# Optimization experiments

Hardware: AMD Instinct MI355X
Metric: run time of the kernel (lower is better)

## Reference

```python
import jax, jax.numpy as jnp
import numpy as np

DIM_IN, DIM_K, DIM_V = 1024, 1024, 1024

def setup_inputs() -> dict:
    key = jax.random.key(0)
    k1, k2, k3, k4 = jax.random.split(key, 4)
    x = jax.random.normal(k1, (4, 2048, DIM_IN), dtype=jnp.float32)
    # Linear(dim_in, dim_k, bias=False): store as [in, out] for x @ W
    Wq = jax.random.normal(k2, (DIM_IN, DIM_K), dtype=jnp.float32) * (1.0 / np.sqrt(DIM_IN))
    Wk = jax.random.normal(k3, (DIM_IN, DIM_K), dtype=jnp.float32) * (1.0 / np.sqrt(DIM_IN))
    Wv = jax.random.normal(k4, (DIM_IN, DIM_V), dtype=jnp.float32) * (1.0 / np.sqrt(DIM_IN))
    return {"x": x, "Wq": Wq, "Wk": Wk, "Wv": Wv, "causal_mask": 1}

def reference(x, Wq, Wk, Wv, causal_mask):
    # x: [b, n, dim_in]
    b, n, _ = x.shape
    q = jnp.einsum('bnd,dk->bnk', x, Wq)
    k = jnp.einsum('bnd,dk->bnk', x, Wk)
    v = jnp.einsum('bnd,dv->bnv', x, Wv)
    scale = 1.0 / np.sqrt(Wq.shape[1])
    dist = jnp.einsum('bik,bjk->bij', q, k) * scale  # [b, n, n]
    if causal_mask:
        mask = jnp.tril(jnp.ones((n, n), dtype=bool))
        dist = jnp.where(mask, dist, -jnp.inf)
    attn = jax.nn.softmax(dist, axis=-1)
    return jnp.einsum('bij,bjv->biv', attn, v)  # [b, n, dim_v]
```

## Files before the change

### kernel.cpp

```cpp
#include <hip/hip_runtime.h>
#include <hip/hip_bf16.h>
#include <stdint.h>

#define BM 128
#define BN 128
#define BK 64

typedef __attribute__((ext_vector_type(8))) short bf16x8;
typedef __attribute__((ext_vector_type(4))) float floatx4;


__device__ __forceinline__ unsigned short f2bf(float f) {
    unsigned int x;
    __builtin_memcpy(&x, &f, 4);
    unsigned int r = (x + 0x7fffu + ((x >> 16) & 1u)) >> 16;
    return (unsigned short)r;
}

__device__ __forceinline__ float bf2f_hi(unsigned int u_hi_masked) {
    float f;
    __builtin_memcpy(&f, &u_hi_masked, 4);
    return f;
}

__device__ __forceinline__ void async_copy16(const void* g, void* l) {
    __builtin_amdgcn_global_load_lds(
        (const __attribute__((address_space(1))) void*)(uintptr_t)g,
        (__attribute__((address_space(3))) void*)(uint32_t)(uintptr_t)l,
        16, 0, 0);
}


__global__ __launch_bounds__(256) void prep(const float* __restrict__ x,
                                            const float* __restrict__ Wq,
                                            const float* __restrict__ Wk,
                                            const float* __restrict__ Wv,
                                            unsigned short* __restrict__ xb,
                                            unsigned short* __restrict__ wT) {
    __shared__ float tile[32][33];
    int bid = blockIdx.x;
    int tid = threadIdx.x;
    if (bid < 8192) {
        int i = bid * 256 + tid;
        float4 v = ((const float4*)x)[i];
        ushort4 o;
        o.x = f2bf(v.x);
        o.y = f2bf(v.y);
        o.z = f2bf(v.z);
        o.w = f2bf(v.w);
        ((ushort4*)xb)[i] = o;
    } else {
        int w = bid - 8192;
        int z = w >> 10;
        int r = w & 1023;
        int bx = (r & 31) * 32;
        int by = (r >> 5) * 32;
        const float* W = z == 0 ? Wq : (z == 1 ? Wk : Wv);
        int tx = tid & 31, ty = tid >> 5;
        for (int rr = 0; rr < 32; rr += 8)
            tile[ty + rr][tx] = W[(size_t)(by + ty + rr) * 1024 + bx + tx];
        __syncthreads();
        unsigned short* o = wT + (size_t)z * 1024 * 1024;
        for (int rr = 0; rr < 32; rr += 8)
            o[(size_t)(bx + ty + rr) * 1024 + by + tx] = f2bf(tile[tx][ty + rr]);
    }
}


#define SEG_STRIDE 544
#define BUF_SH (16 * SEG_STRIDE)


__device__ __forceinline__ void gemm_core(const unsigned short* __restrict__ A,
                                          int lda,
                                          const unsigned short* __restrict__ B,
                                          int ldb, void* __restrict__ C,
                                          int ldc, bool out_bf16, int kend,
                                          float scale, int m0, int n0) {
    __shared__ __align__(16) unsigned short As[BUF_SH];
    __shared__ __align__(16) unsigned short Bs[BUF_SH];

    int tid = threadIdx.x;
    int lane = tid & 63;
    int wave = tid >> 6;
    int wm = (wave >> 1) * 64;
    int wn = (wave & 1) * 64;
    int fr = lane & 15;
    int kq = lane >> 4;

    floatx4 acc[4][4] = {};

    for (int k0 = 0; k0 < kend; k0 += BK) {
#pragma unroll
        for (int q = 0; q < 4; q++) {
            int s = 4 * q + wave;
            int r = s * 8 + (lane >> 3);
            int ko = (lane & 7) * 8;
            int dst = s * SEG_STRIDE + lane * 8;
            async_copy16(A + (size_t)(m0 + r) * lda + k0 + ko, &As[dst]);
            async_copy16(B + (size_t)(n0 + r) * ldb + k0 + ko, &Bs[dst]);
        }
        __syncthreads();

#pragma unroll
        for (int kh = 0; kh < 2; kh++) {
            int kc = kh * 4 + kq;
            bf16x8 af[4], bfg[4];
#pragma unroll
            for (int mi = 0; mi < 4; mi++) {
                int row = wm + mi * 16 + fr;
                af[mi] = *(const bf16x8*)&As[(row >> 3) * SEG_STRIDE +
                                             (row & 7) * 64 + kc * 8];
            }
#pragma unroll
            for (int ni = 0; ni < 4; ni++) {
                int row = wn + ni * 16 + fr;
                bfg[ni] = *(const bf16x8*)&Bs[(row >> 3) * SEG_STRIDE +
                                              (row & 7) * 64 + kc * 8];
            }
#pragma unroll
            for (int mi = 0; mi < 4; mi++)
#pragma unroll
                for (int ni = 0; ni < 4; ni++)
                    acc[mi][ni] = __builtin_amdgcn_mfma_f32_16x16x32_bf16(
                        af[mi], bfg[ni], acc[mi][ni], 0, 0, 0);
        }
        __syncthreads();
    }

    int col0 = n0 + wn + fr;
    int rbase = m0 + wm + kq * 4;
    if (out_bf16) {
        unsigned short* Cb = (unsigned short*)C;
#pragma unroll
        for (int mi = 0; mi < 4; mi++)
#pragma unroll
            for (int ni = 0; ni < 4; ni++)
#pragma unroll
                for (int r = 0; r < 4; r++)
                    Cb[(size_t)(rbase + mi * 16 + r) * ldc + col0 + ni * 16] =
                        f2bf(acc[mi][ni][r] * scale);
    } else {
        float* Cb = (float*)C;
#pragma unroll
        for (int mi = 0; mi < 4; mi++)
#pragma unroll
            for (int ni = 0; ni < 4; ni++)
#pragma unroll
                for (int r = 0; r < 4; r++)
                    Cb[(size_t)(rbase + mi * 16 + r) * ldc + col0 + ni * 16] =
                        acc[mi][ni][r] * scale;
    }
}


__device__ __forceinline__ void gemm_core_db(
    const unsigned short* __restrict__ A, int lda,
    const unsigned short* __restrict__ B, int ldb, void* __restrict__ C,
    int ldc, bool out_bf16, int kend, float scale, int m0, int n0) {
    __shared__ __align__(16) unsigned short As[2 * BUF_SH];
    __shared__ __align__(16) unsigned short Bs[2 * BUF_SH];

    int tid = threadIdx.x;
    int lane = tid & 63;
    int wave = tid >> 6;
    int wm = (wave >> 1) * 64;
    int wn = (wave & 1) * 64;
    int fr = lane & 15;
    int kq = lane >> 4;

    floatx4 acc[4][4] = {};

    auto stage = [&](int buf, int k0) {
#pragma unroll
        for (int q = 0; q < 4; q++) {
            int s = 4 * q + wave;
            int r = s * 8 + (lane >> 3);
            int ko = (lane & 7) * 8;
            int dst = buf * BUF_SH + s * SEG_STRIDE + lane * 8;
            async_copy16(A + (size_t)(m0 + r) * lda + k0 + ko, &As[dst]);
            async_copy16(B + (size_t)(n0 + r) * ldb + k0 + ko, &Bs[dst]);
        }
    };

    auto compute = [&](int buf) {
        const unsigned short* as = &As[buf * BUF_SH];
        const unsigned short* bs = &Bs[buf * BUF_SH];
#pragma unroll
        for (int kh = 0; kh < 2; kh++) {
            int kc = kh * 4 + kq;
            bf16x8 af[4], bfg[4];
#pragma unroll
            for (int mi = 0; mi < 4; mi++) {
                int row = wm + mi * 16 + fr;
                af[mi] = *(const bf16x8*)&as[(row >> 3) * SEG_STRIDE +
                                             (row & 7) * 64 + kc * 8];
            }
#pragma unroll
            for (int ni = 0; ni < 4; ni++) {
                int row = wn + ni * 16 + fr;
                bfg[ni] = *(const bf16x8*)&bs[(row >> 3) * SEG_STRIDE +
                                              (row & 7) * 64 + kc * 8];
            }
#pragma unroll
            for (int mi = 0; mi < 4; mi++)
#pragma unroll
                for (int ni = 0; ni < 4; ni++)
                    acc[mi][ni] = __builtin_amdgcn_mfma_f32_16x16x32_bf16(
                        af[mi], bfg[ni], acc[mi][ni], 0, 0, 0);
        }
    };

    stage(0, 0);
    __syncthreads();
    int nt = kend / BK;
    int cur = 0;
    for (int t = 0; t < nt; t++) {
        if (t + 1 < nt) stage(cur ^ 1, (t + 1) * BK);
        compute(cur);
        __syncthreads();
        cur ^= 1;
    }

    int col0 = n0 + wn + fr;
    int rbase = m0 + wm + kq * 4;
    if (out_bf16) {
        unsigned short* Cb = (unsigned short*)C;
#pragma unroll
        for (int mi = 0; mi < 4; mi++)
#pragma unroll
            for (int ni = 0; ni < 4; ni++)
#pragma unroll
                for (int r = 0; r < 4; r++)
                    Cb[(size_t)(rbase + mi * 16 + r) * ldc + col0 + ni * 16] =
                        f2bf(acc[mi][ni][r] * scale);
    } else {
        float* Cb = (float*)C;
#pragma unroll
        for (int mi = 0; mi < 4; mi++)
#pragma unroll
            for (int ni = 0; ni < 4; ni++)
#pragma unroll
                for (int r = 0; r < 4; r++)
                    Cb[(size_t)(rbase + mi * 16 + r) * ldc + col0 + ni * 16] =
                        acc[mi][ni][r] * scale;
    }
}


__global__ __launch_bounds__(512, 2) void gemm_qk8(
    const unsigned short* __restrict__ A, const unsigned short* __restrict__ B,
    unsigned short* __restrict__ C) {
    __shared__ __align__(16) unsigned short lds[4][16384];

    const int tid = threadIdx.x;
    const int lane = tid & 63;
    const int wave = tid >> 6;
    const int wr = wave >> 2;
    const int wc = wave & 3;
    const int fr = lane & 15;
    const int kq = lane >> 4;
    const int m0 = blockIdx.y * 256;
    const int n0 = blockIdx.x * 256;

    const unsigned short* aS0 =
        A + (size_t)(m0 + wave * 32 + (lane >> 2)) * 1024 + (lane & 3) * 8;
    const unsigned short* aS1 = aS0 + 16 * 1024;
    const unsigned short* bS0 =
        B + (size_t)(n0 + wave * 32 + (lane >> 2)) * 1024 + (lane & 3) * 8;
    const unsigned short* bS1 = bS0 + 16 * 1024;
    const int dA0 = wave * 1024 + lane * 8;
    const int dA1 = dA0 + 512;
    const int dB0 = 8192 + dA0;
    const int dB1 = 8192 + dA1;

    floatx4 acc[8][4] = {};

    auto stageA = [&](int j) {
        unsigned short* d = &lds[j & 3][0];
        int kk = j * 32;
        async_copy16(aS0 + kk, d + dA0);
        async_copy16(aS1 + kk, d + dA1);
    };
    auto stageB = [&](int j) {
        unsigned short* d = &lds[j & 3][0];
        int kk = j * 32;
        async_copy16(bS0 + kk, d + dB0);
        async_copy16(bS1 + kk, d + dB1);
    };

    stageA(0); stageB(0);
    stageA(1); stageB(1);
    stageA(2); stageB(2);

    for (int j = 0; j < 32; ++j) {
        if (j < 30) {
            asm volatile("s_waitcnt vmcnt(8)" ::: "memory");
        } else if (j == 30) {
            asm volatile("s_waitcnt vmcnt(4)" ::: "memory");
        } else {
            asm volatile("s_waitcnt vmcnt(0)" ::: "memory");
        }
        asm volatile("s_barrier" ::: "memory");

        const unsigned short* as = &lds[j & 3][0];
        const unsigned short* bs = as + 8192;
        bf16x8 af[4], bfr[4];

#pragma unroll
        for (int mi = 0; mi < 4; mi++)
            af[mi] = *(const bf16x8*)&as[(wr * 128 + mi * 16 + fr) * 32 + kq * 8];
#pragma unroll
        for (int ni = 0; ni < 4; ni++)
            bfr[ni] = *(const bf16x8*)&bs[(wc * 64 + ni * 16 + fr) * 32 + kq * 8];
        if (j + 3 < 32) stageA(j + 3);
        __builtin_amdgcn_s_setprio(1);
#pragma unroll
        for (int mi = 0; mi < 4; mi++)
#pragma unroll
            for (int ni = 0; ni < 4; ni++)
                acc[mi][ni] = __builtin_amdgcn_mfma_f32_16x16x32_bf16(
                    af[mi], bfr[ni], acc[mi][ni], 0, 0, 0);
        __builtin_amdgcn_s_setprio(0);

#pragma unroll
        for (int mi = 0; mi < 4; mi++)
            af[mi] = *(const bf16x8*)&as[(wr * 128 + 64 + mi * 16 + fr) * 32 +
                                         kq * 8];
#pragma unroll
        for (int ni = 0; ni < 4; ni++)
            bfr[ni] = *(const bf16x8*)&bs[(wc * 64 + ni * 16 + fr) * 32 + kq * 8];
        if (j + 3 < 32) stageB(j + 3);
        __builtin_amdgcn_s_setprio(1);
#pragma unroll
        for (int mi = 0; mi < 4; mi++)
#pragma unroll
            for (int ni = 0; ni < 4; ni++)
                acc[4 + mi][ni] = __builtin_amdgcn_mfma_f32_16x16x32_bf16(
                    af[mi], bfr[ni], acc[4 + mi][ni], 0, 0, 0);
        __builtin_amdgcn_s_setprio(0);
    }

    const int col0 = n0 + wc * 64 + fr;
    const int rbase = m0 + wr * 128 + kq * 4;
#pragma unroll
    for (int a = 0; a < 8; a++)
#pragma unroll
        for (int ni = 0; ni < 4; ni++)
#pragma unroll
            for (int r = 0; r < 4; r++)
                C[(size_t)(rbase + a * 16 + r) * 2048 + col0 + ni * 16] =
                    f2bf(acc[a][ni][r]);
}


__device__ __forceinline__ void tri_decode(int r2, int& mb, int& nb) {
    mb = (int)((sqrtf(8.0f * r2 + 1.0f) - 1.0f) * 0.5f);
    while ((mb + 1) * (mb + 2) / 2 <= r2) mb++;
    while (mb * (mb + 1) / 2 > r2) mb--;
    nb = r2 - mb * (mb + 1) / 2;
}


__global__ __launch_bounds__(256, 4) void gemm_s(
    const unsigned short* __restrict__ qk, unsigned short* __restrict__ S) {
    int bz = blockIdx.x / 136;
    int mb, nb;
    tri_decode(blockIdx.x - bz * 136, mb, nb);
    const unsigned short* Q = qk + (size_t)bz * 2048 * 2048;
    gemm_core(Q, 2048, Q + 1024, 2048, S + (size_t)bz * 2048 * 2048, 2048,
              true, 1024, 0.03125f, mb * BM, nb * BN);
}


__global__ __launch_bounds__(256, 4) void sm_vt(
    unsigned short* __restrict__ S, const unsigned short* __restrict__ wTv,
    const unsigned short* __restrict__ xb, unsigned short* __restrict__ vt) {
    int bid = blockIdx.x;
    if (bid < 512) {
        gemm_core_db(wTv, 1024, xb, 1024, vt, 8192, true, 1024, 1.0f,
                     (bid >> 6) * BM, (bid & 63) * BN);
        return;
    }
    int lane = threadIdx.x & 63;
    int row = (bid - 512) * 4 + (threadIdx.x >> 6);
    int i = row & 2047;
    unsigned short* s = S + (size_t)row * 2048;

    uint4 raw[4];
#pragma unroll
    for (int c = 0; c < 4; c++) raw[c] = ((const uint4*)s)[lane + c * 64];

    const float NEG = -1.0e30f;
    float p[32];
    float m = NEG;
#pragma unroll
    for (int c = 0; c < 4; c++) {
        const unsigned int* u = (const unsigned int*)&raw[c];
#pragma unroll
        for (int w = 0; w < 4; w++) {
            int j = c * 512 + lane * 8 + w * 2;
            float f0 = bf2f_hi(u[w] << 16);
            float f1 = bf2f_hi(u[w] & 0xffff0000u);
            f0 = (j <= i) ? f0 : NEG;
            f1 = (j + 1 <= i) ? f1 : NEG;
            p[c * 8 + w * 2] = f0;
            p[c * 8 + w * 2 + 1] = f1;
            m = fmaxf(m, fmaxf(f0, f1));
        }
    }
#pragma unroll
    for (int o = 32; o > 0; o >>= 1) m = fmaxf(m, __shfl_xor(m, o));

    float sum = 0.f;
#pragma unroll
    for (int t = 0; t < 32; t++) {
        p[t] = __expf(p[t] - m);
        sum += p[t];
    }
#pragma unroll
    for (int o = 32; o > 0; o >>= 1) sum += __shfl_xor(sum, o);
    float inv = 1.0f / sum;

#pragma unroll
    for (int c = 0; c < 4; c++) {
        uint4 out;
        unsigned int* u = (unsigned int*)&out;
#pragma unroll
        for (int w = 0; w < 4; w++) {
            unsigned int lo = f2bf(p[c * 8 + w * 2] * inv);
            unsigned int hi = f2bf(p[c * 8 + w * 2 + 1] * inv);
            u[w] = lo | (hi << 16);
        }
        ((uint4*)s)[lane + c * 64] = out;
    }
}


__global__ __launch_bounds__(256, 4) void gemm_pv(
    const unsigned short* __restrict__ S, const unsigned short* __restrict__ vt,
    float* __restrict__ out) {
    int b = blockIdx.x;
    int j = b < 256 ? b : 767 - b;
    int mb = j >> 5;
    int rem = j & 31;
    int bz = rem >> 3, nb = rem & 7;
    int kend = (mb + 1) * 128;
    gemm_core_db(S + (size_t)bz * 2048 * 2048, 2048, vt + (size_t)bz * 2048,
                 8192, out + (size_t)bz * 2048 * 1024, 1024, false, kend, 1.0f,
                 mb * BM, nb * BN);
}


extern "C" void kernel_launch(void* const* d_in, const int* in_sizes, int n_in,
                              void* d_out, int out_size, void* d_ws,
                              size_t ws_size, hipStream_t stream) {
    const float* x = (const float*)d_in[0];
    const float* Wq = (const float*)d_in[1];
    const float* Wk = (const float*)d_in[2];
    const float* Wv = (const float*)d_in[3];

    char* ws = (char*)d_ws;
    unsigned short* qk = (unsigned short*)(ws);
    unsigned short* S = (unsigned short*)(ws + 33554432);
    unsigned short* vt = (unsigned short*)(ws + 67108864);
    unsigned short* xb = (unsigned short*)(ws + 83886080);
    unsigned short* wT = (unsigned short*)(ws + 100663296);

    prep<<<11264, 256, 0, stream>>>(x, Wq, Wk, Wv, xb, wT);
    gemm_qk8<<<dim3(8, 32), 512, 0, stream>>>(xb, wT, qk);
    gemm_s<<<544, 256, 0, stream>>>(qk, S);
    sm_vt<<<2560, 256, 0, stream>>>(S, wT + 2 * 1024 * 1024, xb, vt);
    gemm_pv<<<512, 256, 0, stream>>>(S, vt, (float*)d_out);
}
```

Measured before the change: 235.3 us.

## Shrink QK projection tile to 128x256 with triple-buffered LDS pipeline

Replaces the 256x256-tile QK projection GEMM with a 128x256 tile, halving per-block accumulators and LDS. The grid doubles to 512 blocks, launch bounds allow 4 blocks per CU, and the pipeline becomes 3-stage with combined A/B staging instead of 4-stage split staging. The goal is more blocks in flight and better CU fill, at the cost of less operand reuse per block and more global traffic for the B matrix.

```diff
diff --git a/kernel.cpp b/kernel.cpp
--- a/kernel.cpp
+++ b/kernel.cpp
@@ -248,10 +248,10 @@
 }
 
 
-__global__ __launch_bounds__(512, 2) void gemm_qk8(
+__global__ __launch_bounds__(512, 4) void gemm_qk2(
     const unsigned short* __restrict__ A, const unsigned short* __restrict__ B,
     unsigned short* __restrict__ C) {
-    __shared__ __align__(16) unsigned short lds[4][16384];
+    __shared__ __align__(16) unsigned short lds[3][12288];
 
     const int tid = threadIdx.x;
     const int lane = tid & 63;
@@ -260,60 +260,50 @@
     const int wc = wave & 3;
     const int fr = lane & 15;
     const int kq = lane >> 4;
-    const int m0 = blockIdx.y * 256;
+    const int m0 = blockIdx.y * 128;
     const int n0 = blockIdx.x * 256;
 
-    const unsigned short* aS0 =
-        A + (size_t)(m0 + wave * 32 + (lane >> 2)) * 1024 + (lane & 3) * 8;
-    const unsigned short* aS1 = aS0 + 16 * 1024;
+    const unsigned short* aS =
+        A + (size_t)(m0 + wave * 16 + (lane >> 2)) * 1024 + (lane & 3) * 8;
     const unsigned short* bS0 =
         B + (size_t)(n0 + wave * 32 + (lane >> 2)) * 1024 + (lane & 3) * 8;
     const unsigned short* bS1 = bS0 + 16 * 1024;
-    const int dA0 = wave * 1024 + lane * 8;
-    const int dA1 = dA0 + 512;
-    const int dB0 = 8192 + dA0;
-    const int dB1 = 8192 + dA1;
-
-    floatx4 acc[8][4] = {};
-
-    auto stageA = [&](int j) {
-        unsigned short* d = &lds[j & 3][0];
+    const int dA = wave * 512 + lane * 8;
+    const int dB0 = 4096 + wave * 1024 + lane * 8;
+    const int dB1 = dB0 + 512;
+
+    floatx4 acc[4][4] = {};
+
+    auto stage = [&](int buf, int j) {
+        unsigned short* d = &lds[buf][0];
         int kk = j * 32;
-        async_copy16(aS0 + kk, d + dA0);
-        async_copy16(aS1 + kk, d + dA1);
-    };
-    auto stageB = [&](int j) {
-        unsigned short* d = &lds[j & 3][0];
-        int kk = j * 32;
+        async_copy16(aS + kk, d + dA);
         async_copy16(bS0 + kk, d + dB0);
         async_copy16(bS1 + kk, d + dB1);
     };
 
-    stageA(0); stageB(0);
-    stageA(1); stageB(1);
-    stageA(2); stageB(2);
-
+    stage(0, 0);
+    stage(1, 1);
+
+    int rbuf = 0, wbuf = 2;
     for (int j = 0; j < 32; ++j) {
-        if (j < 30) {
-            asm volatile("s_waitcnt vmcnt(8)" ::: "memory");
-        } else if (j == 30) {
-            asm volatile("s_waitcnt vmcnt(4)" ::: "memory");
+        if (j < 31) {
+            asm volatile("s_waitcnt vmcnt(3)" ::: "memory");
         } else {
             asm volatile("s_waitcnt vmcnt(0)" ::: "memory");
         }
         asm volatile("s_barrier" ::: "memory");
 
-        const unsigned short* as = &lds[j & 3][0];
-        const unsigned short* bs = as + 8192;
+        const unsigned short* as = &lds[rbuf][0];
+        const unsigned short* bs = as + 4096;
         bf16x8 af[4], bfr[4];
-
-#pragma unroll
-        for (int mi = 0; mi < 4; mi++)
-            af[mi] = *(const bf16x8*)&as[(wr * 128 + mi * 16 + fr) * 32 + kq * 8];
+#pragma unroll
+        for (int mi = 0; mi < 4; mi++)
+            af[mi] = *(const bf16x8*)&as[(wr * 64 + mi * 16 + fr) * 32 + kq * 8];
 #pragma unroll
         for (int ni = 0; ni < 4; ni++)
             bfr[ni] = *(const bf16x8*)&bs[(wc * 64 + ni * 16 + fr) * 32 + kq * 8];
-        if (j + 3 < 32) stageA(j + 3);
+        if (j + 2 < 32) stage(wbuf, j + 2);
         __builtin_amdgcn_s_setprio(1);
 #pragma unroll
         for (int mi = 0; mi < 4; mi++)
@@ -323,34 +313,20 @@
                     af[mi], bfr[ni], acc[mi][ni], 0, 0, 0);
         __builtin_amdgcn_s_setprio(0);
 
-#pragma unroll
-        for (int mi = 0; mi < 4; mi++)
-            af[mi] = *(const bf16x8*)&as[(wr * 128 + 64 + mi * 16 + fr) * 32 +
-                                         kq * 8];
+        rbuf = (rbuf == 2) ? 0 : rbuf + 1;
+        wbuf = (wbuf == 2) ? 0 : wbuf + 1;
+    }
+
+    const int col0 = n0 + wc * 64 + fr;
+    const int rbase = m0 + wr * 64 + kq * 4;
+#pragma unroll
+    for (int mi = 0; mi < 4; mi++)
 #pragma unroll
         for (int ni = 0; ni < 4; ni++)
-            bfr[ni] = *(const bf16x8*)&bs[(wc * 64 + ni * 16 + fr) * 32 + kq * 8];
-        if (j + 3 < 32) stageB(j + 3);
-        __builtin_amdgcn_s_setprio(1);
-#pragma unroll
-        for (int mi = 0; mi < 4; mi++)
-#pragma unroll
-            for (int ni = 0; ni < 4; ni++)
-                acc[4 + mi][ni] = __builtin_amdgcn_mfma_f32_16x16x32_bf16(
-                    af[mi], bfr[ni], acc[4 + mi][ni], 0, 0, 0);
-        __builtin_amdgcn_s_setprio(0);
-    }
-
-    const int col0 = n0 + wc * 64 + fr;
-    const int rbase = m0 + wr * 128 + kq * 4;
-#pragma unroll
-    for (int a = 0; a < 8; a++)
-#pragma unroll
-        for (int ni = 0; ni < 4; ni++)
 #pragma unroll
             for (int r = 0; r < 4; r++)
-                C[(size_t)(rbase + a * 16 + r) * 2048 + col0 + ni * 16] =
-                    f2bf(acc[a][ni][r]);
+                C[(size_t)(rbase + mi * 16 + r) * 2048 + col0 + ni * 16] =
+                    f2bf(acc[mi][ni][r]);
 }
 
 
@@ -468,7 +444,7 @@
     unsigned short* wT = (unsigned short*)(ws + 100663296);
 
     prep<<<11264, 256, 0, stream>>>(x, Wq, Wk, Wv, xb, wT);
-    gemm_qk8<<<dim3(8, 32), 512, 0, stream>>>(xb, wT, qk);
+    gemm_qk2<<<dim3(8, 64), 512, 0, stream>>>(xb, wT, qk);
     gemm_s<<<544, 256, 0, stream>>>(qk, S);
     sm_vt<<<2560, 256, 0, stream>>>(S, wT + 2 * 1024 * 1024, xb, vt);
     gemm_pv<<<512, 256, 0, stream>>>(S, vt, (float*)d_out);
```

New measurement: 236.0 us. No clear change (+0.3%).
